# Kernel optimization log

Hardware: AMD Instinct MI355X
Metric: run time of the kernel (lower is better)

The kernel has to match this reference:

```python
import math
import jax, jax.numpy as jnp
import numpy as np

B, T, C, H = 2, 2048, 1024, 16
D = C // H


def _slopes(n):
    def p2(m):
        start = 2 ** (-(2 ** -(math.log2(m) - 3)))
        return [start * start ** i for i in range(m)]
    if math.log2(n).is_integer():
        return p2(n)
    c = 2 ** math.floor(math.log2(n))
    return p2(c) + _slopes(2 * c)[0::2][: n - c]


def setup_inputs() -> dict:
    key = jax.random.key(0)
    ks = jax.random.split(key, 9)
    std = 0.02
    x = jax.random.normal(ks[0], (B, T, C), dtype=jnp.float32)
    Wq = std * jax.random.normal(ks[1], (C, C), dtype=jnp.float32)
    Wk = std * jax.random.normal(ks[2], (C, C), dtype=jnp.float32)
    Wv = std * jax.random.normal(ks[3], (C, C), dtype=jnp.float32)
    # fc_resid init: std 0.02/sqrt(num_layers)
    Wo = (std / math.sqrt(24.0)) * jax.random.normal(ks[4], (C, C), dtype=jnp.float32)
    bq = jnp.zeros((C,), jnp.float32)
    bk = jnp.zeros((C,), jnp.float32)
    bv = jnp.zeros((C,), jnp.float32)
    bo = jnp.zeros((C,), jnp.float32)
    return {"x": x, "Wq": Wq, "bq": bq, "Wk": Wk, "bk": bk,
            "Wv": Wv, "bv": bv, "Wo": Wo, "bo": bo}


def reference(x, Wq, bq, Wk, bk, Wv, bv, Wo, bo):
    # projections -> [B, T, H, D]
    q = (x @ Wq + bq).reshape(B, T, H, D)
    k = (x @ Wk + bk).reshape(B, T, H, D)
    v = (x @ Wv + bv).reshape(B, T, H, D)

    scale = 1.0 / math.sqrt(D)
    att = jnp.einsum("bqhd,bkhd->bhqk", q, k) * scale  # [B,H,T,T]

    slopes = jnp.asarray(_slopes(H), dtype=jnp.float32)  # [H]
    i = jnp.arange(T)
    rel = i[None, :] - i[None, :].T  # rel[i,j] = j - i
    causal = rel <= 0  # j <= i
    # alibi bias: -tril(i - j) = tril(j - i), scaled per head
    alibi = slopes[:, None, None] * jnp.where(causal, rel, 0).astype(jnp.float32)

    att = att + alibi[None]  # broadcast over batch
    att = jnp.where(causal[None, None], att, -jnp.inf)
    att = jax.nn.softmax(att, axis=-1)

    y = jnp.einsum("bhqk,bkhd->bqhd", att, v).reshape(B, T, C)
    return y @ Wo + bo  # dropout p=0 (eval) is identity
```

## Files before the change

### kernel.cpp

```cpp
#include <hip/hip_runtime.h>
#include <hip/hip_bf16.h>

typedef __bf16 bf16;
typedef __bf16 bf16x4 __attribute__((ext_vector_type(4)));
typedef __bf16 bf16x8 __attribute__((ext_vector_type(8)));
typedef float floatx4 __attribute__((ext_vector_type(4)));
typedef short short4_ __attribute__((ext_vector_type(4)));

#define B_ 2
#define T_ 2048
#define C_ 1024
#define H_ 16
#define D_ 64
#define M_ 4096
#define QK_LD 2048

__device__ __forceinline__ void load_lds16(const void* g, void* l) {
  __builtin_amdgcn_global_load_lds(
      (const __attribute__((address_space(1))) unsigned int*)g,
      (__attribute__((address_space(3))) unsigned int*)l, 16, 0, 0);
}

__device__ __forceinline__ floatx4 mfma16(bf16x4 a, bf16x4 b, floatx4 c) {
#if __has_builtin(__builtin_amdgcn_mfma_f32_16x16x16_bf16)
  return __builtin_amdgcn_mfma_f32_16x16x16_bf16(a, b, c, 0, 0, 0);
#else
  return __builtin_amdgcn_mfma_f32_16x16x16bf16_1k(
      __builtin_bit_cast(short4_, a), __builtin_bit_cast(short4_, b), c, 0, 0, 0);
#endif
}

__device__ __forceinline__ bf16x4 lo4(bf16x8 v) {
  return __builtin_shufflevector(v, v, 0, 1, 2, 3);
}
__device__ __forceinline__ bf16x4 hi4(bf16x8 v) {
  return __builtin_shufflevector(v, v, 4, 5, 6, 7);
}

struct PrepArgs { const float* w[4]; bf16* wt[4]; const float* x; bf16* xb; };

__global__ __launch_bounds__(256)
void prep(PrepArgs p) {
  const int bid = blockIdx.x;
  if (bid < 4096) {
    __shared__ float tile[32][33];
    const int z = bid >> 10, xy = bid & 1023;
    const int bx = xy & 31, by = xy >> 5;
    const float* in = p.w[z];
    bf16* out = p.wt[z];
    int tx = threadIdx.x & 31, ty = threadIdx.x >> 5;
    int n0 = bx * 32, k0 = by * 32;
#pragma unroll
    for (int j = 0; j < 32; j += 8)
      tile[ty + j][tx] = in[(size_t)(k0 + ty + j) * C_ + n0 + tx];
    __syncthreads();
#pragma unroll
    for (int j = 0; j < 32; j += 8)
      out[(size_t)(n0 + ty + j) * C_ + k0 + tx] = (bf16)tile[tx][ty + j];
  } else {
    int i = ((bid - 4096) * 256 + threadIdx.x) * 8;
    float4 a = *(const float4*)(p.x + i);
    float4 b = *(const float4*)(p.x + i + 4);
    bf16x8 o;
    o[0] = (bf16)a.x; o[1] = (bf16)a.y; o[2] = (bf16)a.z; o[3] = (bf16)a.w;
    o[4] = (bf16)b.x; o[5] = (bf16)b.y; o[6] = (bf16)b.z; o[7] = (bf16)b.w;
    *(bf16x8*)(p.xb + i) = o;
  }
}

struct GQ {
  const bf16* A; const bf16* Bt;
  const float* bias[3];
  bf16* Cout; bf16* vt; int N; int K;
};

__global__ __launch_bounds__(256, 2)
void gemm128(GQ g) {
  __shared__ __align__(16) bf16 As[128 * 64];
  __shared__ __align__(16) bf16 Bs[128 * 64];
  const int tid = threadIdx.x;
  const int wave = tid >> 6, lane = tid & 63;
  const int quad = lane >> 4, l16 = lane & 15;
  const int m0 = blockIdx.y * 128, n0 = blockIdx.x * 128;
  const int wm = (wave >> 1) * 64, wn = (wave & 1) * 64;

  floatx4 acc[4][4] = {};

  int rA[4], cA[4];
#pragma unroll
  for (int t = 0; t < 4; ++t) {
    int pch = (wave * 4 + t) * 64 + lane;
    rA[t] = pch >> 3;
    cA[t] = (pch & 7) ^ (rA[t] & 7);
  }

  for (int k0 = 0; k0 < g.K; k0 += 64) {
    __syncthreads();
#pragma unroll
    for (int t = 0; t < 4; ++t) {
      load_lds16(g.A + (size_t)(m0 + rA[t]) * g.K + k0 + cA[t] * 8,
                 As + (wave * 4 + t) * 512);
      load_lds16(g.Bt + (size_t)(n0 + rA[t]) * g.K + k0 + cA[t] * 8,
                 Bs + (wave * 4 + t) * 512);
    }
    __builtin_amdgcn_s_waitcnt(0x0f70);
    __syncthreads();
#pragma unroll
    for (int s = 0; s < 2; ++s) {
      bf16x8 af[4], bfr[4];
#pragma unroll
      for (int i = 0; i < 4; ++i) {
        int mr = wm + i * 16 + l16;
        af[i] = *(const bf16x8*)(As + ((mr * 8) + ((s * 4 + quad) ^ (mr & 7))) * 8);
        int nr = wn + i * 16 + l16;
        bfr[i] = *(const bf16x8*)(Bs + ((nr * 8) + ((s * 4 + quad) ^ (nr & 7))) * 8);
      }
#pragma unroll
      for (int i = 0; i < 4; ++i)
#pragma unroll
        for (int j = 0; j < 4; ++j)
          acc[i][j] = __builtin_amdgcn_mfma_f32_16x16x32_bf16(af[i], bfr[j],
                                                              acc[i][j], 0, 0, 0);
    }
  }

  const bool vsplit = (n0 >= 2048);
#pragma unroll
  for (int j = 0; j < 4; ++j) {
    int col = n0 + wn + j * 16 + l16;
    const float* bp = g.bias[col >> 10];
    float bv = bp[col & 1023];
    if (vsplit) {
      int cv = col - 2048;
      bf16* dstb = g.vt + ((size_t)((m0 >> 11) * 16 + (cv >> 6)) * 64 + (cv & 63)) * (size_t)T_
                   + (m0 & 2047) + wm + quad * 8;
#pragma unroll
      for (int i = 0; i < 4; ++i) {
        bf16x4 pk;
#pragma unroll
        for (int r = 0; r < 4; ++r) pk[r] = (bf16)(acc[i][j][r] + bv);
        *(bf16x4*)(dstb + (i >> 1) * 32 + (i & 1) * 4) = pk;
      }
    } else {
#pragma unroll
      for (int i = 0; i < 4; ++i) {
#pragma unroll
        for (int r = 0; r < 4; ++r) {
          int row = m0 + wm + i * 16 + quad * 4 + r;
          g.Cout[(size_t)row * g.N + col] = (bf16)(acc[i][j][r] + bv);
        }
      }
    }
  }
}

__global__ __launch_bounds__(256, 2)
void gemm_out(const bf16* __restrict__ A, const bf16* __restrict__ Bt,
              const float* __restrict__ bias, float* __restrict__ C) {
  __shared__ __align__(16) bf16 As[64 * 64];
  __shared__ __align__(16) bf16 Bs[128 * 64];
  const int tid = threadIdx.x;
  const int wave = tid >> 6, lane = tid & 63;
  const int quad = lane >> 4, l16 = lane & 15;
  const int m0 = blockIdx.y * 64, n0 = blockIdx.x * 128;
  const int wm = (wave >> 1) * 32, wn = (wave & 1) * 64;

  floatx4 acc[2][4] = {};

  int rA[2], cA[2], rB[4], cB[4];
#pragma unroll
  for (int t = 0; t < 2; ++t) {
    int p = t * 256 + tid;
    rA[t] = p >> 3; cA[t] = (p & 7) ^ (rA[t] & 7);
  }
#pragma unroll
  for (int t = 0; t < 4; ++t) {
    int p = t * 256 + tid;
    rB[t] = p >> 3; cB[t] = (p & 7) ^ (rB[t] & 7);
  }

  for (int k0 = 0; k0 < 1024; k0 += 64) {
    __syncthreads();
#pragma unroll
    for (int t = 0; t < 2; ++t)
      load_lds16(A + (size_t)(m0 + rA[t]) * 1024 + k0 + cA[t] * 8,
                 As + t * 2048 + wave * 512);
#pragma unroll
    for (int t = 0; t < 4; ++t)
      load_lds16(Bt + (size_t)(n0 + rB[t]) * 1024 + k0 + cB[t] * 8,
                 Bs + t * 2048 + wave * 512);
    __builtin_amdgcn_s_waitcnt(0x0f70);
    __syncthreads();
#pragma unroll
    for (int s = 0; s < 2; ++s) {
      bf16x8 af[2], bfr[4];
#pragma unroll
      for (int i = 0; i < 2; ++i) {
        int mr = wm + i * 16 + l16;
        af[i] = *(const bf16x8*)(As + ((mr * 8) + ((s * 4 + quad) ^ (mr & 7))) * 8);
      }
#pragma unroll
      for (int j = 0; j < 4; ++j) {
        int nr = wn + j * 16 + l16;
        bfr[j] = *(const bf16x8*)(Bs + ((nr * 8) + ((s * 4 + quad) ^ (nr & 7))) * 8);
      }
#pragma unroll
      for (int i = 0; i < 2; ++i)
#pragma unroll
        for (int j = 0; j < 4; ++j)
          acc[i][j] = __builtin_amdgcn_mfma_f32_16x16x32_bf16(af[i], bfr[j],
                                                              acc[i][j], 0, 0, 0);
    }
  }

#pragma unroll
  for (int j = 0; j < 4; ++j) {
    int col = n0 + wn + j * 16 + l16;
    float bv = bias[col];
#pragma unroll
    for (int i = 0; i < 2; ++i)
#pragma unroll
      for (int r = 0; r < 4; ++r) {
        int row = m0 + wm + i * 16 + quad * 4 + r;
        C[(size_t)row * 1024 + col] = acc[i][j][r] + bv;
      }
  }
}

__constant__ int yy_map[24] = {7, 8, 16, 9, 17, 6, 10, 18, 11, 19, 5, 12,
                               20, 13, 21, 4, 14, 22, 15, 23, 3, 2, 1, 0};

__global__ __launch_bounds__(512, 2)
void attn8(const bf16* __restrict__ qk, const bf16* __restrict__ vt,
           bf16* __restrict__ y, bf16* __restrict__ po, float* __restrict__ pl) {
  __shared__ __align__(16) bf16 smem[32768];
  const int tid = threadIdx.x, wave = tid >> 6, lane = tid & 63;
  const int quad = lane >> 4, l16 = lane & 15;
  const int qs = wave >> 1, kh = wave & 1;
  const int bh = blockIdx.x, b = bh >> 4, h = bh & 15;
  const int yy = yy_map[blockIdx.y];
  int qb, kbeg, kcnt, seg;
  if (yy < 8)       { qb = yy;      kbeg = 0;      kcnt = 2 * qb + 2; seg = -1; }
  else if (yy < 16) { qb = 23 - yy; kbeg = 0;      kcnt = qb + 1;     seg = 0;  }
  else              { qb = 31 - yy; kbeg = qb + 1; kcnt = qb + 1;     seg = 1;  }

  const float L2E = 1.4426950408889634f;
  const float slope2 = exp2f(-0.5f * (float)(h + 1)) * L2E;
  const float scl2 = 0.125f * L2E;
  const float M0 = 14.0f;

  const int rS = tid >> 3;
  const int cS = (tid & 7) ^ (rS & 7);
  const bf16* kbase = qk + (size_t)b * T_ * QK_LD + 1024 + h * 64;
  const bf16* vbase = vt + (size_t)bh * 64 * T_;

  const int q0 = qb * 128;
  const int w0 = q0 + qs * 32;

  bf16x8 qf[2][2];
#pragma unroll
  for (int qt = 0; qt < 2; ++qt)
#pragma unroll
    for (int s = 0; s < 2; ++s)
      qf[qt][s] = *(const bf16x8*)(qk +
          (size_t)(b * T_ + w0 + qt * 16 + l16) * QK_LD + h * 64 + s * 32 + quad * 8);

  const int qi0 = w0 + l16;
  float qoff[2];
  qoff[0] = slope2 * (float)qi0 + M0;
  qoff[1] = qoff[0] + slope2 * 16.0f;
  float kc[2][4];
#pragma unroll
  for (int kt = 0; kt < 2; ++kt)
#pragma unroll
    for (int r = 0; r < 4; ++r)
      kc[kt][r] = slope2 * (float)(kt * 16 + quad * 4 + r);

  floatx4 o[2][4];
#pragma unroll
  for (int qt = 0; qt < 2; ++qt)
#pragma unroll
    for (int n = 0; n < 4; ++n) o[qt][n] = (floatx4)0.f;
  float lsum[2] = {0.f, 0.f};

#pragma unroll
  for (int s2 = 0; s2 < 2; ++s2) {
    load_lds16(kbase + (size_t)((kbeg + s2) * 64 + rS) * QK_LD + cS * 8,
               smem + s2 * 4096 + wave * 512);
    load_lds16(vbase + (size_t)rS * T_ + (kbeg + s2) * 64 + cS * 8,
               smem + 16384 + s2 * 4096 + wave * 512);
  }
  __builtin_amdgcn_s_waitcnt(0x0f70);
  __syncthreads();

  const int nit = (kcnt + 1) >> 1;
  for (int it = 0; it < nit; ++it) {
    const int cur = it & 1;

    if (it + 1 < nit) {
      const int nt0 = kbeg + 2 * it + 2;
#pragma unroll
      for (int s2 = 0; s2 < 2; ++s2) {
        load_lds16(kbase + (size_t)((nt0 + s2) * 64 + rS) * QK_LD + cS * 8,
                   smem + (cur ^ 1) * 8192 + s2 * 4096 + wave * 512);
        load_lds16(vbase + (size_t)rS * T_ + (nt0 + s2) * 64 + cS * 8,
                   smem + 16384 + (cur ^ 1) * 8192 + s2 * 4096 + wave * 512);
      }
    }

#pragma unroll
    for (int sub = 0; sub < 2; ++sub) {
      const int tile = 2 * it + sub;
      if (tile < kcnt) {
        const int kj0 = (kbeg + tile) * 64;
        const bf16* Klc = smem + cur * 8192 + sub * 4096;
        const bf16* Vlc = smem + 16384 + cur * 8192 + sub * 4096;

        bf16x8 kf[2][2];
#pragma unroll
        for (int ss = 0; ss < 2; ++ss)
#pragma unroll
          for (int kt = 0; kt < 2; ++kt) {
            const int krow = kh * 32 + kt * 16 + l16;
            kf[ss][kt] = *(const bf16x8*)(Klc + krow * 64 +
                                          (((ss * 4 + quad) ^ (krow & 7)) * 8));
          }
        bf16x8 vf8[4];
#pragma unroll
        for (int nt = 0; nt < 4; ++nt) {
          const int drow = nt * 16 + l16;
          vf8[nt] = *(const bf16x8*)(Vlc + drow * 64 +
                                     (((kh * 4 + quad) ^ (drow & 7)) * 8));
        }

        const int kbi = kj0 + kh * 32;
        const float kb = slope2 * (float)kbi;

        __builtin_amdgcn_s_setprio(1);
#pragma unroll
        for (int qt = 0; qt < 2; ++qt) {
          const int rb = w0 + qt * 16;
          floatx4 st[2] = {};
#pragma unroll
          for (int ss = 0; ss < 2; ++ss)
#pragma unroll
            for (int kt = 0; kt < 2; ++kt)
              st[kt] = __builtin_amdgcn_mfma_f32_16x16x32_bf16(kf[ss][kt], qf[qt][ss],
                                                               st[kt], 0, 0, 0);

          const float bb = kb - qoff[qt];
          const int qi = qi0 + qt * 16;
          bf16x4 pb[2];
          if (kbi + 31 > rb) {
#pragma unroll
            for (int kt = 0; kt < 2; ++kt) {
#pragma unroll
              for (int r = 0; r < 4; ++r) {
                float p = __builtin_amdgcn_exp2f(
                    fmaf(st[kt][r], scl2, bb + kc[kt][r]));
                if (kbi + kt * 16 + quad * 4 + r > qi) p = 0.f;
                lsum[qt] += p;
                pb[kt][r] = (bf16)p;
              }
            }
          } else {
#pragma unroll
            for (int kt = 0; kt < 2; ++kt) {
#pragma unroll
              for (int r = 0; r < 4; ++r) {
                float p = __builtin_amdgcn_exp2f(
                    fmaf(st[kt][r], scl2, bb + kc[kt][r]));
                lsum[qt] += p;
                pb[kt][r] = (bf16)p;
              }
            }
          }

#pragma unroll
          for (int nt = 0; nt < 4; ++nt) {
            o[qt][nt] = mfma16(lo4(vf8[nt]), pb[0], o[qt][nt]);
            o[qt][nt] = mfma16(hi4(vf8[nt]), pb[1], o[qt][nt]);
          }
        }
        __builtin_amdgcn_s_setprio(0);
      }
    }

    __builtin_amdgcn_s_waitcnt(0x0f70);
    __syncthreads();
  }

  float* Cb = (float*)smem;
  if (kh == 1) {
#pragma unroll
    for (int qt = 0; qt < 2; ++qt) {
#pragma unroll
      for (int n = 0; n < 4; ++n)
        *(floatx4*)(Cb + (((qs * 2 + qt) * 4 + n) * 64 + lane) * 4) = o[qt][n];
      Cb[8192 + (qs * 2 + qt) * 64 + lane] = lsum[qt];
    }
  }
  __syncthreads();
  if (kh == 1) return;
#pragma unroll
  for (int qt = 0; qt < 2; ++qt) {
#pragma unroll
    for (int n = 0; n < 4; ++n)
      o[qt][n] += *(const floatx4*)(Cb + (((qs * 2 + qt) * 4 + n) * 64 + lane) * 4);
    lsum[qt] += Cb[8192 + (qs * 2 + qt) * 64 + lane];
    lsum[qt] += __shfl_xor(lsum[qt], 16);
    lsum[qt] += __shfl_xor(lsum[qt], 32);
  }

  if (seg < 0) {
#pragma unroll
    for (int qt = 0; qt < 2; ++qt) {
      const float inv = 1.f / lsum[qt];
      bf16* yp = y + (size_t)(b * T_ + w0 + qt * 16 + l16) * C_ + h * 64 + quad * 4;
#pragma unroll
      for (int nt = 0; nt < 4; ++nt) {
        bf16x4 pk;
#pragma unroll
        for (int r = 0; r < 4; ++r) pk[r] = (bf16)(o[qt][nt][r] * inv);
        *(bf16x4*)(yp + nt * 16) = pk;
      }
    }
  } else {
    const int pid = (bh * 8 + (qb - 8)) * 2 + seg;
    bf16* pob = po + (size_t)pid * 8192;
#pragma unroll
    for (int qt = 0; qt < 2; ++qt) {
#pragma unroll
      for (int half = 0; half < 2; ++half) {
        bf16x8 pk;
#pragma unroll
        for (int jj = 0; jj < 8; ++jj)
          pk[jj] = (bf16)o[qt][half * 2 + (jj >> 2)][jj & 3];
        *(bf16x8*)(pob + (qt * 2 + half) * 2048 + (qs * 64 + lane) * 8) = pk;
      }
      if (quad == 0)
        pl[pid * 128 + qs * 32 + qt * 16 + l16] = lsum[qt];
    }
  }
}

__global__ __launch_bounds__(256)
void combine(const bf16* __restrict__ po, const float* __restrict__ pl,
             bf16* __restrict__ y) {
  const int x = blockIdx.x;
  const int bh = x >> 3, qb = (x & 7) + 8;
  const int b = bh >> 4, h = bh & 15;
  const int pid0 = (bh * 8 + (qb - 8)) * 2;
  const bf16* p0 = po + (size_t)pid0 * 8192;
  const bf16* p1 = p0 + 8192;
  const int t = threadIdx.x;
  const int qs = t >> 6, quad = (t >> 4) & 3, l16 = t & 15;

  float linv[2];
  int row[2];
#pragma unroll
  for (int qt = 0; qt < 2; ++qt) {
    row[qt] = qs * 32 + qt * 16 + l16;
    linv[qt] = 1.f / (pl[pid0 * 128 + row[qt]] + pl[(pid0 + 1) * 128 + row[qt]]);
  }

#pragma unroll
  for (int qt = 0; qt < 2; ++qt)
#pragma unroll
    for (int half = 0; half < 2; ++half) {
      bf16x8 a = *(const bf16x8*)(p0 + (qt * 2 + half) * 2048 + t * 8);
      bf16x8 c = *(const bf16x8*)(p1 + (qt * 2 + half) * 2048 + t * 8);
#pragma unroll
      for (int g = 0; g < 2; ++g) {
        bf16x4 outv;
#pragma unroll
        for (int r = 0; r < 4; ++r)
          outv[r] = (bf16)(((float)a[g * 4 + r] + (float)c[g * 4 + r]) * linv[qt]);
        const int col = (half * 2 + g) * 16 + quad * 4;
        *(bf16x4*)(y + (size_t)(b * T_ + qb * 128 + row[qt]) * C_ + h * 64 + col) = outv;
      }
    }
}

extern "C" void kernel_launch(void* const* d_in, const int* in_sizes, int n_in,
                              void* d_out, int out_size, void* d_ws, size_t ws_size,
                              hipStream_t stream) {
  const float* x  = (const float*)d_in[0];
  const float* Wq = (const float*)d_in[1];
  const float* bq = (const float*)d_in[2];
  const float* Wk = (const float*)d_in[3];
  const float* bk = (const float*)d_in[4];
  const float* Wv = (const float*)d_in[5];
  const float* bv = (const float*)d_in[6];
  const float* Wo = (const float*)d_in[7];
  const float* bo = (const float*)d_in[8];

  bf16* ws  = (bf16*)d_ws;
  bf16* WtQ = ws;
  bf16* WtK = WtQ + (size_t)C_ * C_;
  bf16* WtV = WtK + (size_t)C_ * C_;
  bf16* WtO = WtV + (size_t)C_ * C_;
  bf16* xb  = WtO + (size_t)C_ * C_;
  bf16* qkb = xb + (size_t)M_ * C_;
  bf16* vtb = qkb + (size_t)M_ * 2 * C_;
  bf16* yb  = vtb + (size_t)M_ * C_;
  bf16* pob = yb + (size_t)M_ * C_;
  float* plb = (float*)(pob + (size_t)512 * 8192);

  PrepArgs pp;
  pp.w[0] = Wq; pp.w[1] = Wk; pp.w[2] = Wv; pp.w[3] = Wo;
  pp.wt[0] = WtQ; pp.wt[1] = WtK; pp.wt[2] = WtV; pp.wt[3] = WtO;
  pp.x = x; pp.xb = xb;
  prep<<<dim3(4096 + M_ * C_ / (256 * 8)), 256, 0, stream>>>(pp);

  GQ gq;
  gq.A = xb; gq.Bt = WtQ;
  gq.bias[0] = bq; gq.bias[1] = bk; gq.bias[2] = bv;
  gq.Cout = qkb; gq.vt = vtb; gq.N = 2 * C_; gq.K = C_;
  gemm128<<<dim3(24, 32), 256, 0, stream>>>(gq);

  attn8<<<dim3(32, 24), 512, 0, stream>>>(qkb, vtb, yb, pob, plb);
  combine<<<dim3(32 * 8), 256, 0, stream>>>(pob, plb, yb);

  gemm_out<<<dim3(8, 64), 256, 0, stream>>>(yb, WtO, bo, (float*)d_out);
}
```

Before: 182.7 us.

## Remap attention blocks across XCDs, peel odd tile, widen V-transpose stores

The attention grid becomes 1D, and the block id is remapped so that consecutive ids on the same XCD share a (batch, head) group while workload heaviness is interleaved. This is meant to improve L2 locality for K/V and balance load across dies. The inner loop drops the per-subtile bounds check by processing full pairs of tiles and peeling a trailing odd tile. The V-transpose epilogue in the QKV GEMM now writes 8-element bf16 vectors instead of 4-element ones.

```diff
diff --git a/kernel.cpp b/kernel.cpp
--- a/kernel.cpp
+++ b/kernel.cpp
@@ -135,11 +135,12 @@
       bf16* dstb = g.vt + ((size_t)((m0 >> 11) * 16 + (cv >> 6)) * 64 + (cv & 63)) * (size_t)T_
                    + (m0 & 2047) + wm + quad * 8;
 #pragma unroll
-      for (int i = 0; i < 4; ++i) {
-        bf16x4 pk;
-#pragma unroll
-        for (int r = 0; r < 4; ++r) pk[r] = (bf16)(acc[i][j][r] + bv);
-        *(bf16x4*)(dstb + (i >> 1) * 32 + (i & 1) * 4) = pk;
+      for (int ii = 0; ii < 2; ++ii) {
+        bf16x8 pk;
+#pragma unroll
+        for (int r = 0; r < 8; ++r)
+          pk[r] = (bf16)(acc[ii * 2 + (r >> 2)][j][r & 3] + bv);
+        *(bf16x8*)(dstb + ii * 32) = pk;
       }
     } else {
 #pragma unroll
@@ -237,8 +238,11 @@
   const int tid = threadIdx.x, wave = tid >> 6, lane = tid & 63;
   const int quad = lane >> 4, l16 = lane & 15;
   const int qs = wave >> 1, kh = wave & 1;
-  const int bh = blockIdx.x, b = bh >> 4, h = bh & 15;
-  const int yy = yy_map[blockIdx.y];
+  const int id = blockIdx.x;
+  const int pos = id >> 3;
+  const int bh = (id & 7) * 4 + (pos & 3);
+  const int b = bh >> 4, h = bh & 15;
+  const int yy = yy_map[pos >> 2];
   int qb, kbeg, kcnt, seg;
   if (yy < 8)       { qb = yy;      kbeg = 0;      kcnt = 2 * qb + 2; seg = -1; }
   else if (yy < 16) { qb = 23 - yy; kbeg = 0;      kcnt = qb + 1;     seg = 0;  }
@@ -283,6 +287,77 @@
     for (int n = 0; n < 4; ++n) o[qt][n] = (floatx4)0.f;
   float lsum[2] = {0.f, 0.f};
 
+  auto tilebody = [&](const bf16* Klc, const bf16* Vlc, int tile) {
+    const int kj0 = (kbeg + tile) * 64;
+    bf16x8 kf[2][2];
+#pragma unroll
+    for (int ss = 0; ss < 2; ++ss)
+#pragma unroll
+      for (int kt = 0; kt < 2; ++kt) {
+        const int krow = kh * 32 + kt * 16 + l16;
+        kf[ss][kt] = *(const bf16x8*)(Klc + krow * 64 +
+                                      (((ss * 4 + quad) ^ (krow & 7)) * 8));
+      }
+    bf16x8 vf8[4];
+#pragma unroll
+    for (int nt = 0; nt < 4; ++nt) {
+      const int drow = nt * 16 + l16;
+      vf8[nt] = *(const bf16x8*)(Vlc + drow * 64 +
+                                 (((kh * 4 + quad) ^ (drow & 7)) * 8));
+    }
+
+    const int kbi = kj0 + kh * 32;
+    const float kb = slope2 * (float)kbi;
+
+    __builtin_amdgcn_s_setprio(1);
+#pragma unroll
+    for (int qt = 0; qt < 2; ++qt) {
+      const int rb = w0 + qt * 16;
+      floatx4 st[2] = {};
+#pragma unroll
+      for (int ss = 0; ss < 2; ++ss)
+#pragma unroll
+        for (int kt = 0; kt < 2; ++kt)
+          st[kt] = __builtin_amdgcn_mfma_f32_16x16x32_bf16(kf[ss][kt], qf[qt][ss],
+                                                           st[kt], 0, 0, 0);
+
+      const float bb = kb - qoff[qt];
+      const int qi = qi0 + qt * 16;
+      bf16x4 pb[2];
+      if (kbi + 31 > rb) {
+#pragma unroll
+        for (int kt = 0; kt < 2; ++kt) {
+#pragma unroll
+          for (int r = 0; r < 4; ++r) {
+            float p = __builtin_amdgcn_exp2f(
+                fmaf(st[kt][r], scl2, bb + kc[kt][r]));
+            if (kbi + kt * 16 + quad * 4 + r > qi) p = 0.f;
+            lsum[qt] += p;
+            pb[kt][r] = (bf16)p;
+          }
+        }
+      } else {
+#pragma unroll
+        for (int kt = 0; kt < 2; ++kt) {
+#pragma unroll
+          for (int r = 0; r < 4; ++r) {
+            float p = __builtin_amdgcn_exp2f(
+                fmaf(st[kt][r], scl2, bb + kc[kt][r]));
+            lsum[qt] += p;
+            pb[kt][r] = (bf16)p;
+          }
+        }
+      }
+
+#pragma unroll
+      for (int nt = 0; nt < 4; ++nt) {
+        o[qt][nt] = mfma16(lo4(vf8[nt]), pb[0], o[qt][nt]);
+        o[qt][nt] = mfma16(hi4(vf8[nt]), pb[1], o[qt][nt]);
+      }
+    }
+    __builtin_amdgcn_s_setprio(0);
+  };
+
 #pragma unroll
   for (int s2 = 0; s2 < 2; ++s2) {
     load_lds16(kbase + (size_t)((kbeg + s2) * 64 + rS) * QK_LD + cS * 8,
@@ -293,8 +368,9 @@
   __builtin_amdgcn_s_waitcnt(0x0f70);
   __syncthreads();
 
+  const int npair = kcnt >> 1;
   const int nit = (kcnt + 1) >> 1;
-  for (int it = 0; it < nit; ++it) {
+  for (int it = 0; it < npair; ++it) {
     const int cur = it & 1;
 
     if (it + 1 < nit) {
@@ -308,85 +384,15 @@
       }
     }
 
-#pragma unroll
-    for (int sub = 0; sub < 2; ++sub) {
-      const int tile = 2 * it + sub;
-      if (tile < kcnt) {
-        const int kj0 = (kbeg + tile) * 64;
-        const bf16* Klc = smem + cur * 8192 + sub * 4096;
-        const bf16* Vlc = smem + 16384 + cur * 8192 + sub * 4096;
-
-        bf16x8 kf[2][2];
-#pragma unroll
-        for (int ss = 0; ss < 2; ++ss)
-#pragma unroll
-          for (int kt = 0; kt < 2; ++kt) {
-            const int krow = kh * 32 + kt * 16 + l16;
-            kf[ss][kt] = *(const bf16x8*)(Klc + krow * 64 +
-                                          (((ss * 4 + quad) ^ (krow & 7)) * 8));
-          }
-        bf16x8 vf8[4];
-#pragma unroll
-        for (int nt = 0; nt < 4; ++nt) {
-          const int drow = nt * 16 + l16;
-          vf8[nt] = *(const bf16x8*)(Vlc + drow * 64 +
-                                     (((kh * 4 + quad) ^ (drow & 7)) * 8));
-        }
-
-        const int kbi = kj0 + kh * 32;
-        const float kb = slope2 * (float)kbi;
-
-        __builtin_amdgcn_s_setprio(1);
-#pragma unroll
-        for (int qt = 0; qt < 2; ++qt) {
-          const int rb = w0 + qt * 16;
-          floatx4 st[2] = {};
-#pragma unroll
-          for (int ss = 0; ss < 2; ++ss)
-#pragma unroll
-            for (int kt = 0; kt < 2; ++kt)
-              st[kt] = __builtin_amdgcn_mfma_f32_16x16x32_bf16(kf[ss][kt], qf[qt][ss],
-                                                               st[kt], 0, 0, 0);
-
-          const float bb = kb - qoff[qt];
-          const int qi = qi0 + qt * 16;
-          bf16x4 pb[2];
-          if (kbi + 31 > rb) {
-#pragma unroll
-            for (int kt = 0; kt < 2; ++kt) {
-#pragma unroll
-              for (int r = 0; r < 4; ++r) {
-                float p = __builtin_amdgcn_exp2f(
-                    fmaf(st[kt][r], scl2, bb + kc[kt][r]));
-                if (kbi + kt * 16 + quad * 4 + r > qi) p = 0.f;
-                lsum[qt] += p;
-                pb[kt][r] = (bf16)p;
-              }
-            }
-          } else {
-#pragma unroll
-            for (int kt = 0; kt < 2; ++kt) {
-#pragma unroll
-              for (int r = 0; r < 4; ++r) {
-                float p = __builtin_amdgcn_exp2f(
-                    fmaf(st[kt][r], scl2, bb + kc[kt][r]));
-                lsum[qt] += p;
-                pb[kt][r] = (bf16)p;
-              }
-            }
-          }
-
-#pragma unroll
-          for (int nt = 0; nt < 4; ++nt) {
-            o[qt][nt] = mfma16(lo4(vf8[nt]), pb[0], o[qt][nt]);
-            o[qt][nt] = mfma16(hi4(vf8[nt]), pb[1], o[qt][nt]);
-          }
-        }
-        __builtin_amdgcn_s_setprio(0);
-      }
-    }
+    tilebody(smem + cur * 8192,        smem + 16384 + cur * 8192,        2 * it);
+    tilebody(smem + cur * 8192 + 4096, smem + 16384 + cur * 8192 + 4096, 2 * it + 1);
 
     __builtin_amdgcn_s_waitcnt(0x0f70);
+    __syncthreads();
+  }
+  if (kcnt & 1) {
+    const int cur = npair & 1;
+    tilebody(smem + cur * 8192, smem + 16384 + cur * 8192, kcnt - 1);
     __syncthreads();
   }
 
@@ -519,7 +525,7 @@
   gq.Cout = qkb; gq.vt = vtb; gq.N = 2 * C_; gq.K = C_;
   gemm128<<<dim3(24, 32), 256, 0, stream>>>(gq);
 
-  attn8<<<dim3(32, 24), 512, 0, stream>>>(qkb, vtb, yb, pob, plb);
+  attn8<<<dim3(768), 512, 0, stream>>>(qkb, vtb, yb, pob, plb);
   combine<<<dim3(32 * 8), 256, 0, stream>>>(pob, plb, yb);
 
   gemm_out<<<dim3(8, 64), 256, 0, stream>>>(yb, WtO, bo, (float*)d_out);
```

After: 175.1 us. -4.2%, faster.
